# Optimization experiments

Measured on AMD Instinct MI355X. Metric: run time of the kernel, lower is better.

The kernel has to match this reference:

```python
import jax, jax.numpy as jnp
import numpy as np

B, T, C, H, S, M = 4, 4096, 1024, 16, 256, 32
D = C // H  # size_head = 64


def setup_inputs() -> dict:
    key = jax.random.key(0)
    ks = jax.random.split(key, 10)
    scale = 1.0 / (C * C)
    return {
        "x_q": jax.random.normal(ks[0], (B, T, C), dtype=jnp.float32),
        "x_r": jax.random.normal(ks[1], (B, T, C), dtype=jnp.float32),
        "y": jax.random.normal(ks[2], (B, T, C), dtype=jnp.float32),
        "Wi": jax.random.normal(ks[3], (C, C), dtype=jnp.float32) * 0.02,
        "bi": jnp.zeros((C,), jnp.float32),
        "Ws": jax.random.normal(ks[4], (S, D), dtype=jnp.float32) * 0.02,
        "bs": jnp.zeros((S,), jnp.float32),
        "temp": jnp.ones((1, H, 1, 1), jnp.float32) / jnp.sqrt(jnp.float32(D)),
        "w_re": jax.random.uniform(ks[5], (H, D, D, M), dtype=jnp.float32) * scale,
        "w_im": jax.random.uniform(ks[6], (H, D, D, M), dtype=jnp.float32) * scale,
        "Wo": jax.random.normal(ks[7], (C, C), dtype=jnp.float32) * 0.02,
        "bo": jnp.zeros((C,), jnp.float32),
    }


def reference(x_q, x_r, y, Wi, bi, Ws, bs, temp, w_re, w_im, Wo, bo):
    b, t, c = x_q.shape
    d = c // H
    # in_proj -> [B, H, T, D]
    tmp = (x_q @ Wi.T + bi).reshape(b, t, H, d).transpose(0, 2, 1, 3)
    # slice logits [B, H, T, S], scaled by learned temperature
    logits = (tmp @ Ws.T + bs) / temp
    # softmax over tokens (n): slice-attention pooling to S virtual points
    z = jnp.einsum('bhnc,bhns->bhsc', tmp, jax.nn.softmax(logits, axis=-2))
    z = z.transpose(0, 1, 3, 2)  # [B, H, D, S]
    n = z.shape[-1]
    z_fft = jnp.fft.rfft(z)  # [B, H, D, S//2+1]
    w = (w_re + 1j * w_im).astype(z_fft.dtype)
    out_m = jnp.einsum('bhix,hiox->bhox', z_fft[..., :M], w)  # [B, H, D, M]
    out_ft = jnp.zeros((b, H, d, n // 2 + 1), dtype=out_m.dtype).at[..., :M].set(out_m)
    out = jnp.fft.irfft(out_ft, n=n)  # [B, H, D, S]
    out = out.transpose(0, 1, 3, 2)  # [B, H, S, D]
    # softmax over slices (g): scatter back to tokens
    out = jnp.einsum('bhgc,bhng->bhnc', out, jax.nn.softmax(logits, axis=-1))
    out = out.transpose(0, 2, 1, 3).reshape(b, t, c)  # merge heads
    return out @ Wo.T + bo
```

## Files before the change

### kernel.cpp

```cpp
#include <hip/hip_runtime.h>
#include <hip/hip_bf16.h>

typedef __attribute__((ext_vector_type(8))) _Float16 half8;
typedef __attribute__((ext_vector_type(4))) _Float16 half4;
typedef __attribute__((ext_vector_type(4))) float f32x4;

#define DEVFN __device__ __forceinline__

constexpr int B_ = 4, T_ = 4096, C_ = 1024, H_ = 16, S_ = 256, M_ = 32, D_ = 64;
constexpr int NT_ = B_ * T_;
constexpr float FSCALE = 65536.0f;
constexpr float TWOPI = 6.283185307179586f;

DEVFN half8 cvt8(const float4 a, const float4 b) {
  half8 h;
  h[0] = (_Float16)a.x; h[1] = (_Float16)a.y; h[2] = (_Float16)a.z; h[3] = (_Float16)a.w;
  h[4] = (_Float16)b.x; h[5] = (_Float16)b.y; h[6] = (_Float16)b.z; h[7] = (_Float16)b.w;
  return h;
}

#define GLD16(gsrc, ldst)                                                        \
  __builtin_amdgcn_global_load_lds(                                              \
      (const __attribute__((address_space(1))) uint32_t*)(gsrc),                 \
      (__attribute__((address_space(3))) uint32_t*)(ldst), 16, 0, 0)

__global__ void k_diag(float* __restrict__ out, float wsz) {
  if (threadIdx.x == 0 && blockIdx.x == 0) out[0] = wsz;
}

__global__ void kw_cvt(const float* __restrict__ src, _Float16* __restrict__ dst, int n) {
  const int i = (blockIdx.x * blockDim.x + threadIdx.x) * 8;
  if (i < n) {
    float4 a = ((const float4*)(src + i))[0];
    float4 b = ((const float4*)(src + i))[1];
    *(half8*)(dst + i) = cvt8(a, b);
  }
}

__global__ void k0_prep(const float* __restrict__ Ws, const float* __restrict__ bs,
                        const float* __restrict__ temp,
                        _Float16* __restrict__ Wsh, float* __restrict__ bsh) {
  const int h = blockIdx.x;
  const int tid = threadIdx.x;
  const float invt = 1.0f / temp[h];
  for (int i = tid; i < S_ * D_; i += 256)
    Wsh[(size_t)h * S_ * D_ + i] = (_Float16)(Ws[i] * invt);
  if (tid < S_) bsh[h * S_ + tid] = bs[tid] * invt;
}

__global__ __launch_bounds__(256) void k1_in_proj(
    const _Float16* __restrict__ Xh, const _Float16* __restrict__ Wih, const float* __restrict__ bi,
    _Float16* __restrict__ tmp_h, _Float16* __restrict__ tmp_hT)
{
  __shared__ _Float16 SMEM[8704];
  _Float16* As = SMEM;
  _Float16* Bs = SMEM + 4096;
  const int tid = threadIdx.x;
  const int orig = blockIdx.y * gridDim.x + blockIdx.x;
  const int wgid = (orig & 7) * 128 + (orig >> 3);
  const int rowBase = (wgid >> 3) * 128;
  const int colBase = (wgid & 7) * 128;
  const int w = tid >> 6, lane = tid & 63;
  const int wr = w >> 1, wc = w & 1;
  const int fr = lane & 15, fg = lane >> 4;
  const int srow0 = w * 16 + (lane >> 2);
  const int srow1 = (4 + w) * 16 + (lane >> 2);
  const int scol  = (lane & 3) * 8;
  const size_t arow0 = (size_t)(rowBase + srow0) * C_ + scol;
  const size_t arow1 = (size_t)(rowBase + srow1) * C_ + scol;
  const size_t brow0 = (size_t)(colBase + srow0) * C_ + scol;
  const size_t brow1 = (size_t)(colBase + srow1) * C_ + scol;
  f32x4 acc[4][4] = {};
  for (int kt = 0; kt < C_; kt += 32) {
    __syncthreads();
    GLD16(Xh  + arow0 + kt, &As[w * 512]);
    GLD16(Xh  + arow1 + kt, &As[(4 + w) * 512]);
    GLD16(Wih + brow0 + kt, &Bs[w * 512]);
    GLD16(Wih + brow1 + kt, &Bs[(4 + w) * 512]);
    __syncthreads();
    half8 a[4], b[4];
#pragma unroll
    for (int i = 0; i < 4; ++i) a[i] = *(const half8*)&As[(wr * 64 + i * 16 + fr) * 32 + fg * 8];
#pragma unroll
    for (int j = 0; j < 4; ++j) b[j] = *(const half8*)&Bs[(wc * 64 + j * 16 + fr) * 32 + fg * 8];
#pragma unroll
    for (int i = 0; i < 4; ++i)
#pragma unroll
      for (int j = 0; j < 4; ++j)
        acc[i][j] = __builtin_amdgcn_mfma_f32_16x16x32_f16(a[i], b[j], acc[i][j], 0, 0, 0);
  }
  const int bb = rowBase >> 12;
  const int tloc = rowBase & (T_ - 1);
#pragma unroll
  for (int i = 0; i < 4; ++i) {
#pragma unroll
    for (int j = 0; j < 4; ++j) {
      const int col = colBase + wc * 64 + j * 16 + fr;
      const int hh = col >> 6, d = col & 63;
      const float bv = bi[col];
      const int t0 = tloc + wr * 64 + i * 16 + fg * 4;
      half4 pk;
#pragma unroll
      for (int r = 0; r < 4; ++r) pk[r] = (_Float16)(acc[i][j][r] + bv);
      *(half4*)&tmp_hT[(((size_t)(bb * H_ + hh)) * D_ + d) * T_ + t0] = pk;
    }
  }
  _Float16 (*Ep)[136] = (_Float16 (*)[136])&SMEM[0];
#pragma unroll
  for (int ph = 0; ph < 2; ++ph) {
    __syncthreads();
    if (wr == ph) {
#pragma unroll
      for (int i = 0; i < 4; ++i)
#pragma unroll
        for (int j = 0; j < 4; ++j) {
          const int col = colBase + wc * 64 + j * 16 + fr;
          const float bv = bi[col];
#pragma unroll
          for (int r = 0; r < 4; ++r)
            Ep[i * 16 + fg * 4 + r][wc * 64 + j * 16 + fr] = (_Float16)(acc[i][j][r] + bv);
        }
    }
    __syncthreads();
#pragma unroll
    for (int h2 = 0; h2 < 2; ++h2) {
      const int hh2 = (colBase >> 6) + h2;
      const size_t base = (((size_t)(bb * H_ + hh2)) * T_ + tloc + ph * 64) * D_;
#pragma unroll
      for (int p = 0; p < 2; ++p) {
        const int idx = p * 256 + tid;
        const int trow = idx >> 3, seg = idx & 7;
        *(half8*)(tmp_h + base + (size_t)trow * D_ + seg * 8) =
            *(const half8*)&Ep[trow][h2 * 64 + seg * 8];
      }
    }
  }
}

__global__ __launch_bounds__(256) void k3_pool(
    const _Float16* __restrict__ tmp_h, const _Float16* __restrict__ tmp_hT,
    const _Float16* __restrict__ Wsh, const float* __restrict__ bsh,
    float* __restrict__ Zpart, float* __restrict__ rowsumP, float* __restrict__ colsumP)
{
  __shared__ _Float16 Es[256][72];
  const int tid = threadIdx.x;
  const int kc = blockIdx.x;
  const int bh = blockIdx.y;
  const int hh = bh & (H_ - 1);
  const int w = tid >> 6, lane = tid & 63;
  const int fr = lane & 15, fg = lane >> 4;
  const size_t tmpB  = (size_t)bh * T_ * D_;
  const size_t tmpTB = (size_t)bh * D_ * T_;
  const _Float16* WshH = Wsh + (size_t)hh * S_ * D_;
  float bsreg[4];
#pragma unroll
  for (int nj = 0; nj < 4; ++nj) bsreg[nj] = bsh[hh * S_ + w * 64 + nj * 16 + fr];
  f32x4 acc2[4][4] = {};
  float cacc[4] = {0.f, 0.f, 0.f, 0.f};
  for (int step = 0; step < 8; ++step) {
    const int t0 = kc * 512 + step * 64;
    f32x4 acc1[4][4] = {};
#pragma unroll
    for (int ks = 0; ks < 2; ++ks) {
      half8 a[4], b[4];
#pragma unroll
      for (int mi = 0; mi < 4; ++mi)
        a[mi] = *(const half8*)(tmp_h + tmpB + (size_t)(t0 + mi * 16 + fr) * D_ + ks * 32 + fg * 8);
#pragma unroll
      for (int nj = 0; nj < 4; ++nj)
        b[nj] = *(const half8*)(WshH + (size_t)(w * 64 + nj * 16 + fr) * D_ + ks * 32 + fg * 8);
#pragma unroll
      for (int mi = 0; mi < 4; ++mi)
#pragma unroll
        for (int nj = 0; nj < 4; ++nj)
          acc1[mi][nj] = __builtin_amdgcn_mfma_f32_16x16x32_f16(a[mi], b[nj], acc1[mi][nj], 0, 0, 0);
    }
#pragma unroll
    for (int mi = 0; mi < 4; ++mi) {
      float rsp[4] = {0.f, 0.f, 0.f, 0.f};
#pragma unroll
      for (int nj = 0; nj < 4; ++nj) {
        half4 p;
        float csp = 0.f;
#pragma unroll
        for (int r = 0; r < 4; ++r) {
          const float e = __expf(acc1[mi][nj][r] + bsreg[nj]);
          p[r] = (_Float16)e;
          rsp[r] += e;
          csp += e;
        }
        cacc[nj] += csp;
        *(half4*)&Es[w * 64 + nj * 16 + fr][mi * 16 + fg * 4] = p;
      }
#pragma unroll
      for (int r = 0; r < 4; ++r) {
        float v = rsp[r];
        v += __shfl_xor(v, 1); v += __shfl_xor(v, 2);
        v += __shfl_xor(v, 4); v += __shfl_xor(v, 8);
        rsp[r] = v;
      }
      if (fr == 0) {
        float4 rv; rv.x = rsp[0]; rv.y = rsp[1]; rv.z = rsp[2]; rv.w = rsp[3];
        *(float4*)&rowsumP[((size_t)(bh * 4 + w)) * T_ + t0 + mi * 16 + fg * 4] = rv;
      }
    }
#pragma unroll
    for (int kt = 0; kt < 2; ++kt) {
      half8 a2[4], b2[4];
#pragma unroll
      for (int mi = 0; mi < 4; ++mi)
        a2[mi] = *(const half8*)&Es[w * 64 + mi * 16 + fr][kt * 32 + fg * 8];
#pragma unroll
      for (int nj = 0; nj < 4; ++nj)
        b2[nj] = *(const half8*)(tmp_hT + tmpTB + (size_t)(nj * 16 + fr) * T_ + t0 + kt * 32 + fg * 8);
#pragma unroll
      for (int mi = 0; mi < 4; ++mi)
#pragma unroll
        for (int nj = 0; nj < 4; ++nj)
          acc2[mi][nj] = __builtin_amdgcn_mfma_f32_16x16x32_f16(a2[mi], b2[nj], acc2[mi][nj], 0, 0, 0);
    }
  }
#pragma unroll
  for (int nj = 0; nj < 4; ++nj) {
    float v = cacc[nj];
    v += __shfl_xor(v, 16); v += __shfl_xor(v, 32);
    if (fg == 0) colsumP[((size_t)bh * 8 + kc) * S_ + w * 64 + nj * 16 + fr] = v;
  }
#pragma unroll
  for (int mi = 0; mi < 4; ++mi)
#pragma unroll
    for (int nj = 0; nj < 4; ++nj)
#pragma unroll
      for (int r = 0; r < 4; ++r)
        Zpart[(((size_t)bh * 8 + kc) * S_ + w * 64 + mi * 16 + fg * 4 + r) * D_ + nj * 16 + fr]
            = acc2[mi][nj][r];
}

__global__ __launch_bounds__(256) void k4a_dft(
    const float* __restrict__ Zpart, const float* __restrict__ colsumP,
    const float* __restrict__ rowsumP,
    float* __restrict__ Fre, float* __restrict__ Fim, float* __restrict__ rowsum)
{
  __shared__ float zsh[256][17];
  __shared__ float csh[256];
  __shared__ float tc[256], ts[256];
  const int tid = threadIdx.x;
  const int ic = blockIdx.x;
  const int bh = blockIdx.y;
#pragma unroll
  for (int q = 0; q < 4; ++q) {
    const int t = ic * 1024 + q * 256 + tid;
    float v = rowsumP[((size_t)(bh * 4 + 0)) * T_ + t]
            + rowsumP[((size_t)(bh * 4 + 1)) * T_ + t]
            + rowsumP[((size_t)(bh * 4 + 2)) * T_ + t]
            + rowsumP[((size_t)(bh * 4 + 3)) * T_ + t];
    rowsum[(size_t)bh * T_ + t] = v;
  }
  {
    const float ang = (float)tid * (TWOPI / 256.0f);
    tc[tid] = cosf(ang); ts[tid] = sinf(ang);
    float c = 0.f;
#pragma unroll
    for (int kc = 0; kc < 8; ++kc) c += colsumP[((size_t)bh * 8 + kc) * S_ + tid];
    csh[tid] = c;
  }
  __syncthreads();
  for (int idx = tid; idx < 256 * 16; idx += 256) {
    const int s = idx >> 4, dd = idx & 15;
    float v = 0.f;
#pragma unroll
    for (int kc = 0; kc < 8; ++kc)
      v += Zpart[(((size_t)bh * 8 + kc) * S_ + s) * D_ + ic * 16 + dd];
    zsh[s][dd] = v / csh[s];
  }
  __syncthreads();
  const int ii = tid >> 4;
  const int mh = tid & 15;
#pragma unroll
  for (int q = 0; q < 2; ++q) {
    const int m = mh + 16 * q;
    float re = 0.f, im = 0.f;
    int k = 0;
    for (int s = 0; s < 256; ++s) {
      const float zv = zsh[s][ii];
      re += zv * tc[k];
      im -= zv * ts[k];
      k = (k + m) & 255;
    }
    Fre[((size_t)bh * D_ + ic * 16 + ii) * M_ + m] = re;
    Fim[((size_t)bh * D_ + ic * 16 + ii) * M_ + m] = im;
  }
}

__global__ __launch_bounds__(256) void k4b_mix(
    const float* __restrict__ Fre, const float* __restrict__ Fim,
    const float* __restrict__ w_re, const float* __restrict__ w_im,
    _Float16* __restrict__ fout_T)
{
  __shared__ _Float16 Fsr[4][64][33];
  __shared__ _Float16 Fsi[4][64][33];
  __shared__ float Gpre[2][4][4][32];
  __shared__ float Gpim[2][4][4][32];
  __shared__ float Gre[4][4][32];
  __shared__ float Gim[4][4][32];
  __shared__ float tc[256], ts[256];
  const int tid = threadIdx.x;
  const int oc = blockIdx.x;
  const int h  = blockIdx.y;
  for (int idx = tid; idx < 4 * 64 * 32; idx += 256) {
    const int b = idx >> 11, rem = idx & 2047, i = rem >> 5, m = rem & 31;
    const size_t off = ((size_t)(b * 16 + h) * D_ + i) * M_ + m;
    Fsr[b][i][m] = (_Float16)Fre[off];
    Fsi[b][i][m] = (_Float16)Fim[off];
  }
  {
    const float ang = (float)tid * (TWOPI / 256.0f);
    tc[tid] = cosf(ang); ts[tid] = sinf(ang);
  }
  __syncthreads();
  {
    const int ih = tid >> 7, o = (tid >> 5) & 3, m = tid & 31;
    float gre[4] = {0,0,0,0}, gim[4] = {0,0,0,0};
    for (int i = ih * 32; i < ih * 32 + 32; ++i) {
      const size_t wo = (((size_t)h * D_ + i) * D_ + oc * 4 + o) * M_ + m;
      const float wre = w_re[wo], wim = w_im[wo];
#pragma unroll
      for (int b = 0; b < 4; ++b) {
        const float fre = (float)Fsr[b][i][m], fim = (float)Fsi[b][i][m];
        gre[b] += fre * wre - fim * wim;
        gim[b] += fre * wim + fim * wre;
      }
    }
#pragma unroll
    for (int b = 0; b < 4; ++b) { Gpre[ih][b][o][m] = gre[b]; Gpim[ih][b][o][m] = gim[b]; }
  }
  __syncthreads();
  for (int idx = tid; idx < 512; idx += 256) {
    const int b = idx >> 7, o = (idx >> 5) & 3, m = idx & 31;
    Gre[b][o][m] = Gpre[0][b][o][m] + Gpre[1][b][o][m];
    Gim[b][o][m] = Gpim[0][b][o][m] + Gpim[1][b][o][m];
  }
  __syncthreads();
  {
    const int b = tid >> 6, o = (tid >> 4) & 3, sc = tid & 15;
    for (int s5 = 0; s5 < 16; ++s5) {
      const int s = sc * 16 + s5;
      float v = Gre[b][o][0];
      int km = s;
#pragma unroll
      for (int m = 1; m < 32; ++m) {
        v += 2.0f * (Gre[b][o][m] * tc[km] - Gim[b][o][m] * ts[km]);
        km = (km + s) & 255;
      }
      fout_T[((size_t)(b * 16 + h) * D_ + oc * 4 + o) * S_ + s] = (_Float16)(v * (FSCALE / 256.0f));
    }
  }
}

__global__ __launch_bounds__(256) void k5_scatter(
    const _Float16* __restrict__ Wsh, const float* __restrict__ bsh,
    const _Float16* __restrict__ fout_T, const float* __restrict__ rowsum,
    _Float16* __restrict__ tmp_io)
{
  __shared__ _Float16 Fs[64][264];
  __shared__ _Float16 Es[64][264];
  __shared__ float bshl[256];
  const int tid = threadIdx.x;
  const int orig = blockIdx.y * gridDim.x + blockIdx.x;
  const int nidx = (orig & 7) * 64 + (orig >> 3);
  const int bh = nidx >> 3;
  const int tcn = nidx & 7;
  const int hh = bh & (H_ - 1);
  const int w = tid >> 6, lane = tid & 63;
  const int fr = lane & 15, fg = lane >> 4;
  {
    const int row = tid >> 2, c0 = (tid & 3) * 64;
    const _Float16* src = fout_T + (size_t)bh * D_ * S_ + (size_t)row * S_ + c0;
#pragma unroll
    for (int q = 0; q < 8; ++q)
      *(half8*)&Fs[row][c0 + q * 8] = ((const half8*)src)[q];
  }
  bshl[tid] = bsh[hh * S_ + tid];
  __syncthreads();
  const _Float16* WshH = Wsh + (size_t)hh * S_ * D_;
  const size_t tmpB = (size_t)bh * T_ * D_ + (size_t)tcn * 512 * D_;
  const int trow = w * 16 + fr;
  half8 bf0, bf1;
  {
    const _Float16* p = tmp_io + tmpB + (size_t)trow * D_ + fg * 8;
    bf0 = *(const half8*)p;
    bf1 = *(const half8*)(p + 32);
  }
  for (int step = 0; step < 8; ++step) {
    {
      f32x4 acc1[8];
#pragma unroll
      for (int mi = 0; mi < 8; ++mi) acc1[mi] = (f32x4){0.f, 0.f, 0.f, 0.f};
#pragma unroll
      for (int mi = 0; mi < 8; ++mi) {
        const half8 a0 = *(const half8*)(WshH + (size_t)(mi * 16 + fr) * D_ + fg * 8);
        acc1[mi] = __builtin_amdgcn_mfma_f32_16x16x32_f16(a0, bf0, acc1[mi], 0, 0, 0);
      }
#pragma unroll
      for (int mi = 0; mi < 8; ++mi) {
        const half8 a1 = *(const half8*)(WshH + (size_t)(mi * 16 + fr) * D_ + 32 + fg * 8);
        acc1[mi] = __builtin_amdgcn_mfma_f32_16x16x32_f16(a1, bf1, acc1[mi], 0, 0, 0);
      }
#pragma unroll
      for (int mi = 0; mi < 8; ++mi) {
        const float4 bv = *(const float4*)&bshl[mi * 16 + fg * 4];
        half4 pk;
        pk[0] = (_Float16)__expf(acc1[mi][0] + bv.x);
        pk[1] = (_Float16)__expf(acc1[mi][1] + bv.y);
        pk[2] = (_Float16)__expf(acc1[mi][2] + bv.z);
        pk[3] = (_Float16)__expf(acc1[mi][3] + bv.w);
        *(half4*)&Es[trow][mi * 16 + fg * 4] = pk;
      }
    }
    {
      f32x4 acc1[8];
#pragma unroll
      for (int mi = 0; mi < 8; ++mi) acc1[mi] = (f32x4){0.f, 0.f, 0.f, 0.f};
#pragma unroll
      for (int mi = 0; mi < 8; ++mi) {
        const half8 a0 = *(const half8*)(WshH + (size_t)((8 + mi) * 16 + fr) * D_ + fg * 8);
        acc1[mi] = __builtin_amdgcn_mfma_f32_16x16x32_f16(a0, bf0, acc1[mi], 0, 0, 0);
      }
#pragma unroll
      for (int mi = 0; mi < 8; ++mi) {
        const half8 a1 = *(const half8*)(WshH + (size_t)((8 + mi) * 16 + fr) * D_ + 32 + fg * 8);
        acc1[mi] = __builtin_amdgcn_mfma_f32_16x16x32_f16(a1, bf1, acc1[mi], 0, 0, 0);
      }
#pragma unroll
      for (int mi = 0; mi < 8; ++mi) {
        const float4 bv = *(const float4*)&bshl[(8 + mi) * 16 + fg * 4];
        half4 pk;
        pk[0] = (_Float16)__expf(acc1[mi][0] + bv.x);
        pk[1] = (_Float16)__expf(acc1[mi][1] + bv.y);
        pk[2] = (_Float16)__expf(acc1[mi][2] + bv.z);
        pk[3] = (_Float16)__expf(acc1[mi][3] + bv.w);
        *(half4*)&Es[trow][(8 + mi) * 16 + fg * 4] = pk;
      }
    }
    if (step < 7) {
      const _Float16* p = tmp_io + tmpB + (size_t)((step + 1) * 64 + trow) * D_ + fg * 8;
      bf0 = *(const half8*)p;
      bf1 = *(const half8*)(p + 32);
    }
    f32x4 acc2[4];
#pragma unroll
    for (int nj = 0; nj < 4; ++nj) acc2[nj] = (f32x4){0.f, 0.f, 0.f, 0.f};
#pragma unroll
    for (int ks = 0; ks < 8; ++ks) {
      const half8 ea = *(const half8*)&Es[w * 16 + fr][ks * 32 + fg * 8];
#pragma unroll
      for (int nj = 0; nj < 4; ++nj) {
        const half8 fb = *(const half8*)&Fs[nj * 16 + fr][ks * 32 + fg * 8];
        acc2[nj] = __builtin_amdgcn_mfma_f32_16x16x32_f16(ea, fb, acc2[nj], 0, 0, 0);
      }
    }
    const int tstep0 = tcn * 512 + step * 64;
    {
      const int tbase = tstep0 + w * 16 + fg * 4;
      const float4 rs = *(const float4*)&rowsum[(size_t)bh * T_ + tbase];
      const float ri[4] = {1.0f / rs.x, 1.0f / rs.y, 1.0f / rs.z, 1.0f / rs.w};
#pragma unroll
      for (int r = 0; r < 4; ++r)
#pragma unroll
        for (int nj = 0; nj < 4; ++nj)
          Es[w * 16 + fg * 4 + r][nj * 16 + fr] = (_Float16)(acc2[nj][r] * ri[r]);
      const int trow8 = lane >> 3, seg = lane & 7;
#pragma unroll
      for (int p = 0; p < 2; ++p) {
        const int rloc = w * 16 + p * 8 + trow8;
        *(half8*)(tmp_io + (size_t)bh * T_ * D_ + (size_t)(tstep0 + rloc) * D_ + seg * 8) =
            *(const half8*)&Es[rloc][seg * 8];
      }
    }
  }
}

__global__ __launch_bounds__(256) void k6_out_proj(
    const _Float16* __restrict__ OT, const _Float16* __restrict__ Woh, const float* __restrict__ bo,
    float* __restrict__ Y)
{
  __shared__ _Float16 As[128 * 32];
  __shared__ _Float16 Bs[128 * 32];
  const int tid = threadIdx.x;
  const int orig = blockIdx.y * gridDim.x + blockIdx.x;
  const int wgid = (orig & 7) * 128 + (orig >> 3);
  const int rowBase = (wgid >> 3) * 128;
  const int colBase = (wgid & 7) * 128;
  const int w = tid >> 6, lane = tid & 63;
  const int wr = w >> 1, wc = w & 1;
  const int fr = lane & 15, fg = lane >> 4;
  const int srow0 = w * 16 + (lane >> 2);
  const int srow1 = (4 + w) * 16 + (lane >> 2);
  const int scol  = (lane & 3) * 8;
  const int g0 = rowBase + srow0, g1 = rowBase + srow1;
  const int bb = g0 >> 12;
  const int t0 = g0 & (T_ - 1), t1 = g1 & (T_ - 1);
  const size_t brow0 = (size_t)(colBase + srow0) * C_ + scol;
  const size_t brow1 = (size_t)(colBase + srow1) * C_ + scol;
  f32x4 acc[4][4] = {};
  for (int kt = 0; kt < C_; kt += 32) {
    const int c0 = kt + scol;
    const int hh0 = c0 >> 6, d0 = c0 & 63;
    __syncthreads();
    GLD16(OT + (((size_t)(bb * H_ + hh0)) * T_ + t0) * D_ + d0, &As[w * 512]);
    GLD16(OT + (((size_t)(bb * H_ + hh0)) * T_ + t1) * D_ + d0, &As[(4 + w) * 512]);
    GLD16(Woh + brow0 + kt, &Bs[w * 512]);
    GLD16(Woh + brow1 + kt, &Bs[(4 + w) * 512]);
    __syncthreads();
    half8 a[4], b[4];
#pragma unroll
    for (int i = 0; i < 4; ++i) a[i] = *(const half8*)&As[(wr * 64 + i * 16 + fr) * 32 + fg * 8];
#pragma unroll
    for (int j = 0; j < 4; ++j) b[j] = *(const half8*)&Bs[(wc * 64 + j * 16 + fr) * 32 + fg * 8];
#pragma unroll
    for (int i = 0; i < 4; ++i)
#pragma unroll
      for (int j = 0; j < 4; ++j)
        acc[i][j] = __builtin_amdgcn_mfma_f32_16x16x32_f16(a[i], b[j], acc[i][j], 0, 0, 0);
  }
#pragma unroll
  for (int i = 0; i < 4; ++i) {
#pragma unroll
    for (int j = 0; j < 4; ++j) {
      const int col = colBase + wc * 64 + j * 16 + fr;
      const float bv = bo[col];
      const int g0o = rowBase + wr * 64 + i * 16 + fg * 4;
#pragma unroll
      for (int r = 0; r < 4; ++r)
        Y[(size_t)(g0o + r) * C_ + col] = acc[i][j][r] * (1.0f / FSCALE) + bv;
    }
  }
}

extern "C" void kernel_launch(void* const* d_in, const int* in_sizes, int n_in,
                              void* d_out, int out_size, void* d_ws, size_t ws_size,
                              hipStream_t stream)
{
  const float* x_q  = (const float*)d_in[0];
  const float* Wi   = (const float*)d_in[3];
  const float* bi   = (const float*)d_in[4];
  const float* Ws   = (const float*)d_in[5];
  const float* bs   = (const float*)d_in[6];
  const float* temp = (const float*)d_in[7];
  const float* w_re = (const float*)d_in[8];
  const float* w_im = (const float*)d_in[9];
  const float* Wo   = (const float*)d_in[10];
  const float* bo   = (const float*)d_in[11];
  float* Y = (float*)d_out;

  char* ws = (char*)d_ws;
  size_t off = 0;
  auto alloc = [&](size_t bytes) { size_t o = off; off += (bytes + 255) & ~(size_t)255; return o; };
  const size_t o_tmp  = alloc((size_t)NT_ * C_ * 2);
  const size_t o_Wsh  = alloc((size_t)H_ * S_ * D_ * 2);
  const size_t o_bsh  = alloc((size_t)H_ * S_ * 4);
  const size_t o_Zp   = alloc((size_t)B_ * H_ * 8 * S_ * D_ * 4);
  const size_t o_row  = alloc((size_t)B_ * H_ * T_ * 4);
  const size_t o_rowP = alloc((size_t)B_ * H_ * 4 * T_ * 4);
  const size_t o_colP = alloc((size_t)B_ * H_ * 8 * S_ * 4);
  const size_t o_Fre  = alloc((size_t)B_ * H_ * D_ * M_ * 4);
  const size_t o_Fim  = alloc((size_t)B_ * H_ * D_ * M_ * 4);
  const size_t o_fout = alloc((size_t)B_ * H_ * D_ * S_ * 2);
  const size_t o_Wih  = alloc((size_t)C_ * C_ * 2);
  const size_t o_Woh  = alloc((size_t)C_ * C_ * 2);
  if (off > ws_size) {
    k_diag<<<1, 64, 0, stream>>>(Y, (float)ws_size);
    return;
  }

  _Float16* tmp    = (_Float16*)(ws + o_tmp);
  _Float16* Wsh    = (_Float16*)(ws + o_Wsh);
  float*    bsh    = (float*)(ws + o_bsh);
  float*    Zpart  = (float*)(ws + o_Zp);
  float*    rowsum = (float*)(ws + o_row);
  float*    rowsumP= (float*)(ws + o_rowP);
  float*    colsumP= (float*)(ws + o_colP);
  float*    Fre    = (float*)(ws + o_Fre);
  float*    Fim    = (float*)(ws + o_Fim);
  _Float16* fout_T = (_Float16*)(ws + o_fout);
  _Float16* Wih    = (_Float16*)(ws + o_Wih);
  _Float16* Woh    = (_Float16*)(ws + o_Woh);
  _Float16* Xh     = (_Float16*)d_out;
  _Float16* tmp_hT = (_Float16*)((char*)d_out + (size_t)NT_ * C_ * 2);

  kw_cvt    <<<dim3(8192),    256, 0, stream>>>(x_q, Xh, NT_ * C_);
  kw_cvt    <<<dim3(512),     256, 0, stream>>>(Wi, Wih, C_ * C_);
  kw_cvt    <<<dim3(512),     256, 0, stream>>>(Wo, Woh, C_ * C_);
  k0_prep   <<<dim3(H_),      256, 0, stream>>>(Ws, bs, temp, Wsh, bsh);
  k1_in_proj<<<dim3(8, 128),  256, 0, stream>>>(Xh, Wih, bi, tmp, tmp_hT);
  k3_pool   <<<dim3(8, B_*H_), 256, 0, stream>>>(tmp, tmp_hT, Wsh, bsh, Zpart, rowsumP, colsumP);
  k4a_dft   <<<dim3(4, B_*H_), 256, 0, stream>>>(Zpart, colsumP, rowsumP, Fre, Fim, rowsum);
  k4b_mix   <<<dim3(16, H_),   256, 0, stream>>>(Fre, Fim, w_re, w_im, fout_T);
  k5_scatter<<<dim3(8, B_*H_), 256, 0, stream>>>(Wsh, bsh, fout_T, rowsum, tmp);
  k6_out_proj<<<dim3(8, 128),  256, 0, stream>>>(tmp, Woh, bo, Y);
}
```

Before: 300.2 us.

## Recompute softmax row sums in scatter kernel and prefetch pool operands

The per-token softmax row sums are no longer written by the pool kernel and reduced in the DFT kernel. The scatter kernel now accumulates them from the exponentials it already computes and reduces them with wave shuffles, which removes the rowsumP and rowsum buffers and their global traffic. The pool kernel also register-double-buffers the tmp_h and tmp_hT operand loads for the next step so they overlap the current MFMA and exp work. This costs more registers, which may reduce occupancy, and relies on the shuffle lane mapping matching the accumulator row layout.

```diff
diff --git a/kernel.cpp b/kernel.cpp
--- a/kernel.cpp
+++ b/kernel.cpp
@@ -140,7 +140,7 @@
 __global__ __launch_bounds__(256) void k3_pool(
     const _Float16* __restrict__ tmp_h, const _Float16* __restrict__ tmp_hT,
     const _Float16* __restrict__ Wsh, const float* __restrict__ bsh,
-    float* __restrict__ Zpart, float* __restrict__ rowsumP, float* __restrict__ colsumP)
+    float* __restrict__ Zpart, float* __restrict__ colsumP)
 {
   __shared__ _Float16 Es[256][72];
   const int tid = threadIdx.x;
@@ -157,15 +157,28 @@
   for (int nj = 0; nj < 4; ++nj) bsreg[nj] = bsh[hh * S_ + w * 64 + nj * 16 + fr];
   f32x4 acc2[4][4] = {};
   float cacc[4] = {0.f, 0.f, 0.f, 0.f};
+  half8 pa[2][4];
+  half8 pb[2][4];
+  {
+    const int t0 = kc * 512;
+#pragma unroll
+    for (int ks = 0; ks < 2; ++ks)
+#pragma unroll
+      for (int mi = 0; mi < 4; ++mi)
+        pa[ks][mi] = *(const half8*)(tmp_h + tmpB + (size_t)(t0 + mi * 16 + fr) * D_ + ks * 32 + fg * 8);
+#pragma unroll
+    for (int kt = 0; kt < 2; ++kt)
+#pragma unroll
+      for (int nj = 0; nj < 4; ++nj)
+        pb[kt][nj] = *(const half8*)(tmp_hT + tmpTB + (size_t)(nj * 16 + fr) * T_ + t0 + kt * 32 + fg * 8);
+  }
   for (int step = 0; step < 8; ++step) {
     const int t0 = kc * 512 + step * 64;
+    const int t1 = t0 + 64;
     f32x4 acc1[4][4] = {};
 #pragma unroll
     for (int ks = 0; ks < 2; ++ks) {
-      half8 a[4], b[4];
-#pragma unroll
-      for (int mi = 0; mi < 4; ++mi)
-        a[mi] = *(const half8*)(tmp_h + tmpB + (size_t)(t0 + mi * 16 + fr) * D_ + ks * 32 + fg * 8);
+      half8 b[4];
 #pragma unroll
       for (int nj = 0; nj < 4; ++nj)
         b[nj] = *(const half8*)(WshH + (size_t)(w * 64 + nj * 16 + fr) * D_ + ks * 32 + fg * 8);
@@ -173,11 +186,17 @@
       for (int mi = 0; mi < 4; ++mi)
 #pragma unroll
         for (int nj = 0; nj < 4; ++nj)
-          acc1[mi][nj] = __builtin_amdgcn_mfma_f32_16x16x32_f16(a[mi], b[nj], acc1[mi][nj], 0, 0, 0);
+          acc1[mi][nj] = __builtin_amdgcn_mfma_f32_16x16x32_f16(pa[ks][mi], b[nj], acc1[mi][nj], 0, 0, 0);
+    }
+    if (step < 7) {
+#pragma unroll
+      for (int ks = 0; ks < 2; ++ks)
+#pragma unroll
+        for (int mi = 0; mi < 4; ++mi)
+          pa[ks][mi] = *(const half8*)(tmp_h + tmpB + (size_t)(t1 + mi * 16 + fr) * D_ + ks * 32 + fg * 8);
     }
 #pragma unroll
     for (int mi = 0; mi < 4; ++mi) {
-      float rsp[4] = {0.f, 0.f, 0.f, 0.f};
 #pragma unroll
       for (int nj = 0; nj < 4; ++nj) {
         half4 p;
@@ -186,38 +205,30 @@
         for (int r = 0; r < 4; ++r) {
           const float e = __expf(acc1[mi][nj][r] + bsreg[nj]);
           p[r] = (_Float16)e;
-          rsp[r] += e;
           csp += e;
         }
         cacc[nj] += csp;
         *(half4*)&Es[w * 64 + nj * 16 + fr][mi * 16 + fg * 4] = p;
       }
-#pragma unroll
-      for (int r = 0; r < 4; ++r) {
-        float v = rsp[r];
-        v += __shfl_xor(v, 1); v += __shfl_xor(v, 2);
-        v += __shfl_xor(v, 4); v += __shfl_xor(v, 8);
-        rsp[r] = v;
-      }
-      if (fr == 0) {
-        float4 rv; rv.x = rsp[0]; rv.y = rsp[1]; rv.z = rsp[2]; rv.w = rsp[3];
-        *(float4*)&rowsumP[((size_t)(bh * 4 + w)) * T_ + t0 + mi * 16 + fg * 4] = rv;
-      }
     }
 #pragma unroll
     for (int kt = 0; kt < 2; ++kt) {
-      half8 a2[4], b2[4];
+      half8 a2[4];
 #pragma unroll
       for (int mi = 0; mi < 4; ++mi)
         a2[mi] = *(const half8*)&Es[w * 64 + mi * 16 + fr][kt * 32 + fg * 8];
 #pragma unroll
-      for (int nj = 0; nj < 4; ++nj)
-        b2[nj] = *(const half8*)(tmp_hT + tmpTB + (size_t)(nj * 16 + fr) * T_ + t0 + kt * 32 + fg * 8);
-#pragma unroll
       for (int mi = 0; mi < 4; ++mi)
 #pragma unroll
         for (int nj = 0; nj < 4; ++nj)
-          acc2[mi][nj] = __builtin_amdgcn_mfma_f32_16x16x32_f16(a2[mi], b2[nj], acc2[mi][nj], 0, 0, 0);
+          acc2[mi][nj] = __builtin_amdgcn_mfma_f32_16x16x32_f16(a2[mi], pb[kt][nj], acc2[mi][nj], 0, 0, 0);
+    }
+    if (step < 7) {
+#pragma unroll
+      for (int kt = 0; kt < 2; ++kt)
+#pragma unroll
+        for (int nj = 0; nj < 4; ++nj)
+          pb[kt][nj] = *(const half8*)(tmp_hT + tmpTB + (size_t)(nj * 16 + fr) * T_ + t1 + kt * 32 + fg * 8);
     }
   }
 #pragma unroll
@@ -238,8 +249,7 @@
 
 __global__ __launch_bounds__(256) void k4a_dft(
     const float* __restrict__ Zpart, const float* __restrict__ colsumP,
-    const float* __restrict__ rowsumP,
-    float* __restrict__ Fre, float* __restrict__ Fim, float* __restrict__ rowsum)
+    float* __restrict__ Fre, float* __restrict__ Fim)
 {
   __shared__ float zsh[256][17];
   __shared__ float csh[256];
@@ -247,15 +257,6 @@
   const int tid = threadIdx.x;
   const int ic = blockIdx.x;
   const int bh = blockIdx.y;
-#pragma unroll
-  for (int q = 0; q < 4; ++q) {
-    const int t = ic * 1024 + q * 256 + tid;
-    float v = rowsumP[((size_t)(bh * 4 + 0)) * T_ + t]
-            + rowsumP[((size_t)(bh * 4 + 1)) * T_ + t]
-            + rowsumP[((size_t)(bh * 4 + 2)) * T_ + t]
-            + rowsumP[((size_t)(bh * 4 + 3)) * T_ + t];
-    rowsum[(size_t)bh * T_ + t] = v;
-  }
   {
     const float ang = (float)tid * (TWOPI / 256.0f);
     tc[tid] = cosf(ang); ts[tid] = sinf(ang);
@@ -359,8 +360,7 @@
 
 __global__ __launch_bounds__(256) void k5_scatter(
     const _Float16* __restrict__ Wsh, const float* __restrict__ bsh,
-    const _Float16* __restrict__ fout_T, const float* __restrict__ rowsum,
-    _Float16* __restrict__ tmp_io)
+    const _Float16* __restrict__ fout_T, _Float16* __restrict__ tmp_io)
 {
   __shared__ _Float16 Fs[64][264];
   __shared__ _Float16 Es[64][264];
@@ -392,6 +392,7 @@
     bf1 = *(const half8*)(p + 32);
   }
   for (int step = 0; step < 8; ++step) {
+    float sumE = 0.f;
     {
       f32x4 acc1[8];
 #pragma unroll
@@ -409,11 +410,14 @@
 #pragma unroll
       for (int mi = 0; mi < 8; ++mi) {
         const float4 bv = *(const float4*)&bshl[mi * 16 + fg * 4];
+        float e0 = __expf(acc1[mi][0] + bv.x);
+        float e1 = __expf(acc1[mi][1] + bv.y);
+        float e2 = __expf(acc1[mi][2] + bv.z);
+        float e3 = __expf(acc1[mi][3] + bv.w);
+        sumE += (e0 + e1) + (e2 + e3);
         half4 pk;
-        pk[0] = (_Float16)__expf(acc1[mi][0] + bv.x);
-        pk[1] = (_Float16)__expf(acc1[mi][1] + bv.y);
-        pk[2] = (_Float16)__expf(acc1[mi][2] + bv.z);
-        pk[3] = (_Float16)__expf(acc1[mi][3] + bv.w);
+        pk[0] = (_Float16)e0; pk[1] = (_Float16)e1;
+        pk[2] = (_Float16)e2; pk[3] = (_Float16)e3;
         *(half4*)&Es[trow][mi * 16 + fg * 4] = pk;
       }
     }
@@ -434,14 +438,19 @@
 #pragma unroll
       for (int mi = 0; mi < 8; ++mi) {
         const float4 bv = *(const float4*)&bshl[(8 + mi) * 16 + fg * 4];
+        float e0 = __expf(acc1[mi][0] + bv.x);
+        float e1 = __expf(acc1[mi][1] + bv.y);
+        float e2 = __expf(acc1[mi][2] + bv.z);
+        float e3 = __expf(acc1[mi][3] + bv.w);
+        sumE += (e0 + e1) + (e2 + e3);
         half4 pk;
-        pk[0] = (_Float16)__expf(acc1[mi][0] + bv.x);
-        pk[1] = (_Float16)__expf(acc1[mi][1] + bv.y);
-        pk[2] = (_Float16)__expf(acc1[mi][2] + bv.z);
-        pk[3] = (_Float16)__expf(acc1[mi][3] + bv.w);
+        pk[0] = (_Float16)e0; pk[1] = (_Float16)e1;
+        pk[2] = (_Float16)e2; pk[3] = (_Float16)e3;
         *(half4*)&Es[trow][(8 + mi) * 16 + fg * 4] = pk;
       }
     }
+    sumE += __shfl_xor(sumE, 16);
+    sumE += __shfl_xor(sumE, 32);
     if (step < 7) {
       const _Float16* p = tmp_io + tmpB + (size_t)((step + 1) * 64 + trow) * D_ + fg * 8;
       bf0 = *(const half8*)p;
@@ -461,9 +470,9 @@
     }
     const int tstep0 = tcn * 512 + step * 64;
     {
-      const int tbase = tstep0 + w * 16 + fg * 4;
-      const float4 rs = *(const float4*)&rowsum[(size_t)bh * T_ + tbase];
-      const float ri[4] = {1.0f / rs.x, 1.0f / rs.y, 1.0f / rs.z, 1.0f / rs.w};
+      float ri[4];
+#pragma unroll
+      for (int r = 0; r < 4; ++r) ri[r] = 1.0f / __shfl(sumE, fg * 4 + r);
 #pragma unroll
       for (int r = 0; r < 4; ++r)
 #pragma unroll
@@ -560,8 +569,6 @@
   const size_t o_Wsh  = alloc((size_t)H_ * S_ * D_ * 2);
   const size_t o_bsh  = alloc((size_t)H_ * S_ * 4);
   const size_t o_Zp   = alloc((size_t)B_ * H_ * 8 * S_ * D_ * 4);
-  const size_t o_row  = alloc((size_t)B_ * H_ * T_ * 4);
-  const size_t o_rowP = alloc((size_t)B_ * H_ * 4 * T_ * 4);
   const size_t o_colP = alloc((size_t)B_ * H_ * 8 * S_ * 4);
   const size_t o_Fre  = alloc((size_t)B_ * H_ * D_ * M_ * 4);
   const size_t o_Fim  = alloc((size_t)B_ * H_ * D_ * M_ * 4);
@@ -577,8 +584,6 @@
   _Float16* Wsh    = (_Float16*)(ws + o_Wsh);
   float*    bsh    = (float*)(ws + o_bsh);
   float*    Zpart  = (float*)(ws + o_Zp);
-  float*    rowsum = (float*)(ws + o_row);
-  float*    rowsumP= (float*)(ws + o_rowP);
   float*    colsumP= (float*)(ws + o_colP);
   float*    Fre    = (float*)(ws + o_Fre);
   float*    Fim    = (float*)(ws + o_Fim);
@@ -593,9 +598,9 @@
   kw_cvt    <<<dim3(512),     256, 0, stream>>>(Wo, Woh, C_ * C_);
   k0_prep   <<<dim3(H_),      256, 0, stream>>>(Ws, bs, temp, Wsh, bsh);
   k1_in_proj<<<dim3(8, 128),  256, 0, stream>>>(Xh, Wih, bi, tmp, tmp_hT);
-  k3_pool   <<<dim3(8, B_*H_), 256, 0, stream>>>(tmp, tmp_hT, Wsh, bsh, Zpart, rowsumP, colsumP);
-  k4a_dft   <<<dim3(4, B_*H_), 256, 0, stream>>>(Zpart, colsumP, rowsumP, Fre, Fim, rowsum);
+  k3_pool   <<<dim3(8, B_*H_), 256, 0, stream>>>(tmp, tmp_hT, Wsh, bsh, Zpart, colsumP);
+  k4a_dft   <<<dim3(4, B_*H_), 256, 0, stream>>>(Zpart, colsumP, Fre, Fim);
   k4b_mix   <<<dim3(16, H_),   256, 0, stream>>>(Fre, Fim, w_re, w_im, fout_T);
-  k5_scatter<<<dim3(8, B_*H_), 256, 0, stream>>>(Wsh, bsh, fout_T, rowsum, tmp);
+  k5_scatter<<<dim3(8, B_*H_), 256, 0, stream>>>(Wsh, bsh, fout_T, tmp);
   k6_out_proj<<<dim3(8, 128),  256, 0, stream>>>(tmp, Woh, bo, Y);
 }
```

Measured after the change: 285.3 us. -5.0%, faster.
